# Performance work log

Measured on AMD Instinct MI355X. Metric: run time of the kernel, lower is better.

The kernel has to match this reference:

```python
import jax, jax.numpy as jnp
import numpy as np

B, CIN, COUT, H, W = 8, 8, 16, 256, 256

def setup_inputs() -> dict:
    key = jax.random.key(0)
    k1, k2, k3 = jax.random.split(key, 3)
    x = jax.random.normal(k1, (B, CIN, H, W), dtype=jnp.float32)
    bin_centers = jax.random.normal(k2, (COUT, CIN), dtype=jnp.float32)
    bin_widths = jax.random.normal(k3, (COUT, CIN), dtype=jnp.float32)
    return {"x": x, "bin_centers": bin_centers, "bin_widths": bin_widths}

def reference(x, bin_centers, bin_widths):
    # Gaussian RBF soft-histogram: hist[b,o,h,w] = sum_j exp(-(x[b,j,h,w]-c[o,j])^2 / (2*w[o,j]^2))
    # Original torch code builds hist but (buggily) returns x; we return hist,
    # the actual computation of interest (the nested-loop accumulation).
    diff = x[:, None, :, :, :] - bin_centers[None, :, :, None, None]      # [B,Cout,Cin,H,W]
    inv_two_var = 1.0 / (2.0 * bin_widths[None, :, :, None, None] ** 2)
    hist = jnp.sum(jnp.exp(-(diff ** 2) * inv_two_var), axis=2)           # [B,Cout,H,W]
    return hist
```

## Files before the change

### kernel.cpp

```cpp
#include <hip/hip_runtime.h>


constexpr int CIN   = 8;
constexpr int COUT  = 16;
constexpr int HW    = 256 * 256;
constexpr int BATCH = 8;

__global__ __launch_bounds__(256, 8) void rbf_hist_kernel(
    const float* __restrict__ x,
    const float* __restrict__ centers,
    const float* __restrict__ widths,
    float* __restrict__ out)
{
    __shared__ float2 s_cn[COUT * CIN];

    const int tid = threadIdx.x;
    if (tid < COUT * CIN) {
        float w = widths[tid];
        float negk = -1.4426950408889634f / (2.0f * w * w);
        s_cn[tid] = make_float2(centers[tid], negk);
    }
    __syncthreads();

    const int t = blockIdx.x * 256 + tid;
    const int b = t >> 16;
    const int p = t & (HW - 1);

    const float* __restrict__ xb = x + (b * CIN) * HW + p;
    float xr[CIN];
#pragma unroll
    for (int j = 0; j < CIN; ++j) {
        xr[j] = xb[j * HW];
    }

    float* __restrict__ ob = out + (b * COUT) * HW + p;

#pragma unroll 2
    for (int o = 0; o < COUT; ++o) {
        float acc = 0.f;
#pragma unroll
        for (int j = 0; j < CIN; ++j) {
            const float2 cn = s_cn[o * CIN + j];
            const float d = xr[j] - cn.x;
            acc += __builtin_amdgcn_exp2f((cn.y * d) * d);
        }
        ob[o * HW] = acc;
    }
}

extern "C" void kernel_launch(void* const* d_in, const int* in_sizes, int n_in,
                              void* d_out, int out_size, void* d_ws, size_t ws_size,
                              hipStream_t stream) {
    const float* x       = (const float*)d_in[0];
    const float* centers = (const float*)d_in[1];
    const float* widths  = (const float*)d_in[2];
    float* out           = (float*)d_out;

    const int total_threads = BATCH * HW;
    const int block = 256;
    const int grid  = total_threads / block;

    rbf_hist_kernel<<<grid, block, 0, stream>>>(x, centers, widths, out);
}
```

Before: 82.92 us.

## Precompute RBF table in prep kernel and process two pixels per thread

Moves the center/coefficient table setup into a separate one-block prep kernel that writes to workspace. The main kernel then reads the table through uniform global (likely scalar) loads instead of shared memory, which removes the shared-memory staging and the block barrier. Each thread now handles two adjacent pixels using float2 loads and stores, halving the thread count and widening memory accesses. The costs are an extra kernel launch, a lower occupancy hint, and higher register use per thread.

Result: no change. 84.49 us (+1.9%).

```diff
diff --git a/kernel.cpp b/kernel.cpp
--- a/kernel.cpp
+++ b/kernel.cpp
@@ -5,46 +5,50 @@
 constexpr int COUT  = 16;
 constexpr int HW    = 256 * 256;
 constexpr int BATCH = 8;
+constexpr int PXT   = 2;
 
-__global__ __launch_bounds__(256, 8) void rbf_hist_kernel(
+__global__ void rbf_prep_kernel(const float* __restrict__ centers,
+                                const float* __restrict__ widths,
+                                float2* __restrict__ tab)
+{
+    const int i = threadIdx.x;
+    if (i < COUT * CIN) {
+        const float w = widths[i];
+        const float negk = -1.4426950408889634f / (2.0f * w * w);
+        tab[i] = make_float2(centers[i], negk);
+    }
+}
+
+__global__ __launch_bounds__(256, 4) void rbf_hist_kernel(
     const float* __restrict__ x,
-    const float* __restrict__ centers,
-    const float* __restrict__ widths,
+    const float2* __restrict__ tab,
     float* __restrict__ out)
 {
-    __shared__ float2 s_cn[COUT * CIN];
+    const int t = blockIdx.x * 256 + threadIdx.x;
+    const int b = t >> 15;
+    const int p = (t & (HW / PXT - 1)) * PXT;
 
-    const int tid = threadIdx.x;
-    if (tid < COUT * CIN) {
-        float w = widths[tid];
-        float negk = -1.4426950408889634f / (2.0f * w * w);
-        s_cn[tid] = make_float2(centers[tid], negk);
-    }
-    __syncthreads();
-
-    const int t = blockIdx.x * 256 + tid;
-    const int b = t >> 16;
-    const int p = t & (HW - 1);
-
-    const float* __restrict__ xb = x + (b * CIN) * HW + p;
-    float xr[CIN];
+    const float* __restrict__ xb = x + (size_t)(b * CIN) * HW + p;
+    float2 xr[CIN];
 #pragma unroll
     for (int j = 0; j < CIN; ++j) {
-        xr[j] = xb[j * HW];
+        xr[j] = *reinterpret_cast<const float2*>(xb + (size_t)j * HW);
     }
 
-    float* __restrict__ ob = out + (b * COUT) * HW + p;
+    float* __restrict__ ob = out + (size_t)(b * COUT) * HW + p;
 
-#pragma unroll 2
+#pragma unroll 4
     for (int o = 0; o < COUT; ++o) {
-        float acc = 0.f;
+        float ax = 0.f, ay = 0.f;
 #pragma unroll
         for (int j = 0; j < CIN; ++j) {
-            const float2 cn = s_cn[o * CIN + j];
-            const float d = xr[j] - cn.x;
-            acc += __builtin_amdgcn_exp2f((cn.y * d) * d);
+            const float2 cn = tab[o * CIN + j];
+            const float d0 = xr[j].x - cn.x;
+            const float d1 = xr[j].y - cn.x;
+            ax += __builtin_amdgcn_exp2f((cn.y * d0) * d0);
+            ay += __builtin_amdgcn_exp2f((cn.y * d1) * d1);
         }
-        ob[o * HW] = acc;
+        *reinterpret_cast<float2*>(ob + (size_t)o * HW) = make_float2(ax, ay);
     }
 }
 
@@ -55,10 +59,12 @@
     const float* centers = (const float*)d_in[1];
     const float* widths  = (const float*)d_in[2];
     float* out           = (float*)d_out;
+    float2* tab          = (float2*)d_ws;
 
-    const int total_threads = BATCH * HW;
+    rbf_prep_kernel<<<1, 128, 0, stream>>>(centers, widths, tab);
+
+    const int total_threads = BATCH * HW / PXT;
     const int block = 256;
     const int grid  = total_threads / block;
-
-    rbf_hist_kernel<<<grid, block, 0, stream>>>(x, centers, widths, out);
+    rbf_hist_kernel<<<grid, block, 0, stream>>>(x, tab, out);
 }
```
